# Performance work log

Hardware: AMD Instinct MI355X
Metric: run time of the kernel (lower is better)

The kernel has to match this reference:

```python
import jax, jax.numpy as jnp
import numpy as np

N_NODES = 1_000_000
N_EDGES = 16_000_000
NUM_REL = 3
C_IN, C_OUT = 3, 2


def setup_inputs() -> dict:
    key = jax.random.key(0)
    ks = jax.random.split(key, 10)
    x = jax.random.normal(ks[0], (N_NODES, C_IN), dtype=jnp.float32)
    edge_index = jax.random.randint(ks[1], (2, N_EDGES), 0, N_NODES, dtype=jnp.int64)
    edge_attr = jax.random.randint(ks[2], (N_EDGES,), 0, NUM_REL, dtype=jnp.int64)
    s = 0.3
    W1 = jax.random.normal(ks[3], (NUM_REL, C_IN, C_OUT), dtype=jnp.float32) * s
    root1 = jax.random.normal(ks[4], (C_IN, C_OUT), dtype=jnp.float32) * s
    b1 = jax.random.normal(ks[5], (C_OUT,), dtype=jnp.float32) * s
    W2 = jax.random.normal(ks[6], (NUM_REL, C_OUT, C_OUT), dtype=jnp.float32) * s
    root2 = jax.random.normal(ks[7], (C_OUT, C_OUT), dtype=jnp.float32) * s
    b2 = jax.random.normal(ks[8], (C_OUT,), dtype=jnp.float32) * s
    return {"x": x, "edge_index": edge_index, "edge_attr": edge_attr,
            "W1": W1, "root1": root1, "b1": b1,
            "W2": W2, "root2": root2, "b2": b2}


def rgcn_conv(x, edge_index, edge_type, W, root, bias, num_nodes):
    """PyG RGCNConv: per-relation mean-aggregated messages + root transform + bias."""
    src, dst = edge_index[0], edge_index[1]
    xs = x[src]                                    # [E, c_in] gather once
    out = x @ root + bias                          # [N, c_out]
    for r in range(NUM_REL):                       # small fixed relation loop
        mask = (edge_type == r)
        msg = jnp.where(mask[:, None], xs @ W[r], 0.0)          # [E, c_out]
        sums = jax.ops.segment_sum(msg, dst, num_segments=num_nodes)
        cnt = jax.ops.segment_sum(mask.astype(x.dtype), dst, num_segments=num_nodes)
        out = out + sums / jnp.maximum(cnt, 1.0)[:, None]       # mean aggr
    return out


def reference(x, edge_index, edge_attr, W1, root1, b1, W2, root2, b2):
    h = rgcn_conv(x, edge_index, edge_attr, W1, root1, b1, N_NODES)
    h = jax.nn.relu(h)
    # F.dropout(training=self.training): identity in eval mode
    out = rgcn_conv(h, edge_index, edge_attr, W2, root2, b2, N_NODES)
    return out
```

## Files before the change

### kernel.cpp

```cpp
#include <hip/hip_runtime.h>


typedef unsigned long long u64;
typedef unsigned u32;
typedef float vfloat2 __attribute__((ext_vector_type(2)));

constexpr int NN = 1000000;
constexpr int NE = 16000000;
constexpr int NR = 3;

constexpr int BSH   = 10;
constexpr int NB    = (NN + 1023) >> 10;
constexpr int BCAP  = 18432;
constexpr int EPB   = 16384;
constexpr int NBLKB = (NE + EPB - 1) / EPB;
constexpr int EPT   = EPB / 1024;

constexpr u64 M28 = (1ULL << 28) - 1;

__device__ __forceinline__ u64 pack_msg(float m0, float m1) {
    int a0 = __float2int_rn(fmaf(m0, 4096.0f, 524288.0f));
    int a1 = __float2int_rn(fmaf(m1, 4096.0f, 524288.0f));
    return (u64)(u32)a0 | ((u64)(u32)a1 << 28) | (1ULL << 56);
}

__device__ __forceinline__ u32 enc_x(float x0, float x1, float x2) {
    int q0 = __float2int_rn(fminf(fmaxf(x0 * 64.0f, -511.0f), 511.0f));
    int q1 = __float2int_rn(fminf(fmaxf(x1 * 128.0f, -1023.0f), 1023.0f));
    int q2 = __float2int_rn(fminf(fmaxf(x2 * 128.0f, -1023.0f), 1023.0f));
    return ((u32)q0 & 0x3FFu) | (((u32)q1 & 0x7FFu) << 10) | (((u32)q2 & 0x7FFu) << 21);
}

__device__ __forceinline__ void dec_x(u32 e, float& x0, float& x1, float& x2) {
    x0 = (float)((int)(e << 22) >> 22) * (1.0f / 64.0f);
    x1 = (float)((int)(e << 11) >> 21) * (1.0f / 128.0f);
    x2 = (float)((int)e >> 21)         * (1.0f / 128.0f);
}

__device__ __forceinline__ u32 enc_h(float h0, float h1) {
    int q0 = __float2int_rn(fminf(h0 * 1024.0f, 32767.0f));
    int q1 = __float2int_rn(fminf(h1 * 1024.0f, 32767.0f));
    return ((u32)q0 & 0xFFFFu) | ((u32)q1 << 16);
}

__device__ __forceinline__ void dec_h(u32 e, float& h0, float& h1) {
    h0 = (float)((int)(e << 16) >> 16) * (1.0f / 1024.0f);
    h1 = (float)((int)e >> 16)         * (1.0f / 1024.0f);
}


__global__ __launch_bounds__(1024, 8) void scatter_kernel(
    const int* __restrict__ src, const int* __restrict__ dst, const int* __restrict__ rel,
    const float* __restrict__ x, u32* __restrict__ qx,
    u32* __restrict__ buf, u32* __restrict__ cursor)
{
    __shared__ u32 stage[EPB];
    __shared__ u32 hist[1024];
    __shared__ u32 wcur[1024];
    __shared__ u32 gbase[1024];
    __shared__ u32 wt[16];
    const int tid = threadIdx.x;
    const int wave = tid >> 6, lane = tid & 63;

    hist[tid] = 0;
    __syncthreads();

    const int base = blockIdx.x * EPB;
    const int nloc = min(EPB, NE - base);

    u32 rent[EPT], rbk[EPT];
#pragma unroll
    for (int k = 0; k < EPT; ++k) {
        int i = tid + (k << 10);
        if (i < nloc) {
            int e = base + i;
            u32 d = (u32)__builtin_nontemporal_load(&dst[e]);
            u32 s = (u32)__builtin_nontemporal_load(&src[e]);
            u32 r = (u32)__builtin_nontemporal_load(&rel[e]);
            rbk[k]  = d >> BSH;
            rent[k] = s | (r << 20) | ((d & 1023u) << 22);
            atomicAdd(&hist[rbk[k]], 1u);
        }
    }
    __syncthreads();

    {
        int h0 = hist[tid];
        int v0 = h0;
#pragma unroll
        for (int d = 1; d < 64; d <<= 1) {
            int t = __shfl_up(v0, d);
            if (lane >= d) v0 += t;
        }
        if (lane == 63) wt[wave] = (u32)v0;
        __syncthreads();
        u32 off = 0;
#pragma unroll
        for (int wv = 0; wv < 16; ++wv) off += (wv < wave) ? wt[wv] : 0u;
        wcur[tid] = off + (u32)(v0 - h0);
    }
    __syncthreads();

    if (tid < NB) {
        u32 c = hist[tid];
        gbase[tid] = c ? atomicAdd(&cursor[tid], c) : 0u;
    }

    {
        int node = (blockIdx.x << BSH) + tid;
        if (node < NN)
            qx[node] = enc_x(x[3 * node + 0], x[3 * node + 1], x[3 * node + 2]);
    }
    __syncthreads();

#pragma unroll
    for (int k = 0; k < EPT; ++k) {
        int i = tid + (k << 10);
        if (i < nloc) {
            u32 sl = atomicAdd(&wcur[rbk[k]], 1u);
            stage[sl] = rent[k];
        }
    }
    __syncthreads();

    for (int b = wave; b < NB; b += 16) {
        u32 cnt = hist[b];
        if (!cnt) continue;
        u32 ls = wcur[b] - cnt;
        u32 gb = gbase[b];
        u32* bb = buf + (size_t)b * BCAP;
        for (u32 j = lane; j < cnt; j += 64) {
            u32 slot = gb + j;
            if (slot < (u32)BCAP)
                __builtin_nontemporal_store(stage[ls + j], &bb[slot]);
        }
    }
}

__global__ __launch_bounds__(512) void agg1_kernel(
    const u32* __restrict__ buf, const u32* __restrict__ cursor,
    const u32* __restrict__ qx, const float* __restrict__ x,
    const float* __restrict__ W1,
    const float* __restrict__ root1, const float* __restrict__ b1,
    u32* __restrict__ qh)
{
    __shared__ u64 acc[1024 * NR];
    __shared__ float w[NR * 3 * 2];
    const int tid = threadIdx.x;
    for (int i = tid; i < 1024 * NR; i += 512) acc[i] = 0;
    if (tid < NR * 3 * 2) w[tid] = W1[tid];
    __syncthreads();

    const int bk = blockIdx.x;
    const int n = min((int)cursor[bk], BCAP);
    const u32* bb = buf + (size_t)bk * BCAP;

    int i = tid;
    for (; i + 3584 < n; i += 4096) {
        u32 e[8], g[8];
#pragma unroll
        for (int j = 0; j < 8; ++j) e[j] = __builtin_nontemporal_load(&bb[i + 512 * j]);
#pragma unroll
        for (int j = 0; j < 8; ++j) g[j] = qx[e[j] & 0xFFFFFu];
#pragma unroll
        for (int j = 0; j < 8; ++j) {
            float a, b, c;
            dec_x(g[j], a, b, c);
            u32 r = (e[j] >> 20) & 3u; const float* wr = &w[r * 6];
            atomicAdd(&acc[(e[j] >> 22) * NR + r],
                pack_msg(a * wr[0] + b * wr[2] + c * wr[4],
                         a * wr[1] + b * wr[3] + c * wr[5]));
        }
    }
    for (; i < n; i += 512) {
        u32 e0 = __builtin_nontemporal_load(&bb[i]);
        u32 g0 = qx[e0 & 0xFFFFFu];
        float a, b, c;
        dec_x(g0, a, b, c);
        u32 r = (e0 >> 20) & 3u; const float* wr = &w[r * 6];
        atomicAdd(&acc[(e0 >> 22) * NR + r],
            pack_msg(a * wr[0] + b * wr[2] + c * wr[4],
                     a * wr[1] + b * wr[3] + c * wr[5]));
    }
    __syncthreads();

    for (int l = tid; l < 1024; l += 512) {
        int node = (bk << BSH) + l;
        if (node >= NN) continue;
        float x0 = x[3 * node + 0], x1 = x[3 * node + 1], x2 = x[3 * node + 2];
        float o0 = x0 * root1[0] + x1 * root1[2] + x2 * root1[4] + b1[0];
        float o1 = x0 * root1[1] + x1 * root1[3] + x2 * root1[5] + b1[1];
#pragma unroll
        for (int r = 0; r < NR; ++r) {
            u64 wv = acc[l * NR + r];
            int c = (int)(wv >> 56);
            int s0i = (int)(wv & M28) - (c << 19);
            int s1i = (int)((wv >> 28) & M28) - (c << 19);
            float inv = (1.0f / 4096.0f) / (float)(c > 1 ? c : 1);
            o0 += (float)s0i * inv;
            o1 += (float)s1i * inv;
        }
        qh[node] = enc_h(fmaxf(o0, 0.0f), fmaxf(o1, 0.0f));
    }
}

__global__ __launch_bounds__(512) void agg2_kernel(
    const u32* __restrict__ buf, const u32* __restrict__ cursor,
    const u32* __restrict__ qh, const float* __restrict__ W2,
    const float* __restrict__ root2, const float* __restrict__ b2,
    float* __restrict__ out)
{
    __shared__ u64 acc[1024 * NR];
    __shared__ float w[NR * 2 * 2];
    const int tid = threadIdx.x;
    for (int i = tid; i < 1024 * NR; i += 512) acc[i] = 0;
    if (tid < NR * 2 * 2) w[tid] = W2[tid];
    __syncthreads();

    const int bk = blockIdx.x;
    const int n = min((int)cursor[bk], BCAP);
    const u32* bb = buf + (size_t)bk * BCAP;

    int i = tid;
    for (; i + 3584 < n; i += 4096) {
        u32 e[8], g[8];
#pragma unroll
        for (int j = 0; j < 8; ++j) e[j] = __builtin_nontemporal_load(&bb[i + 512 * j]);
#pragma unroll
        for (int j = 0; j < 8; ++j) g[j] = qh[e[j] & 0xFFFFFu];
#pragma unroll
        for (int j = 0; j < 8; ++j) {
            float a, b;
            dec_h(g[j], a, b);
            u32 r = (e[j] >> 20) & 3u; const float* wr = &w[r * 4];
            atomicAdd(&acc[(e[j] >> 22) * NR + r],
                pack_msg(a * wr[0] + b * wr[2], a * wr[1] + b * wr[3]));
        }
    }
    for (; i < n; i += 512) {
        u32 e0 = __builtin_nontemporal_load(&bb[i]);
        u32 g0 = qh[e0 & 0xFFFFFu];
        float a, b;
        dec_h(g0, a, b);
        u32 r = (e0 >> 20) & 3u; const float* wr = &w[r * 4];
        atomicAdd(&acc[(e0 >> 22) * NR + r],
            pack_msg(a * wr[0] + b * wr[2], a * wr[1] + b * wr[3]));
    }
    __syncthreads();

    for (int l = tid; l < 1024; l += 512) {
        int node = (bk << BSH) + l;
        if (node >= NN) continue;
        float hv0, hv1;
        dec_h(qh[node], hv0, hv1);
        float o0 = hv0 * root2[0] + hv1 * root2[2] + b2[0];
        float o1 = hv0 * root2[1] + hv1 * root2[3] + b2[1];
#pragma unroll
        for (int r = 0; r < NR; ++r) {
            u64 wv = acc[l * NR + r];
            int c = (int)(wv >> 56);
            int s0i = (int)(wv & M28) - (c << 19);
            int s1i = (int)((wv >> 28) & M28) - (c << 19);
            float inv = (1.0f / 4096.0f) / (float)(c > 1 ? c : 1);
            o0 += (float)s0i * inv;
            o1 += (float)s1i * inv;
        }
        vfloat2 ov;
        ov.x = o0; ov.y = o1;
        __builtin_nontemporal_store(ov, (vfloat2*)((float2*)out + node));
    }
}


__global__ __launch_bounds__(256) void edge1_kernel(
    const int* __restrict__ src, const int* __restrict__ dst, const int* __restrict__ rel,
    const float* __restrict__ x, const float* __restrict__ W1,
    u64* __restrict__ sums1)
{
    __shared__ float w[NR * 3 * 2];
    if (threadIdx.x < NR * 3 * 2) w[threadIdx.x] = W1[threadIdx.x];
    __syncthreads();
    int e = blockIdx.x * 256 + threadIdx.x;
    if (e >= NE) return;
    int s = src[e], d = dst[e], r = rel[e];
    float x0 = x[3 * s + 0], x1 = x[3 * s + 1], x2 = x[3 * s + 2];
    const float* wr = &w[r * 6];
    float m0 = x0 * wr[0] + x1 * wr[2] + x2 * wr[4];
    float m1 = x0 * wr[1] + x1 * wr[3] + x2 * wr[5];
    atomicAdd(&sums1[d * NR + r], pack_msg(m0, m1));
}

__global__ __launch_bounds__(256) void node1_kernel(
    const float* __restrict__ x, const u64* __restrict__ sums1,
    const float* __restrict__ root1, const float* __restrict__ b1,
    float* __restrict__ h)
{
    int n = blockIdx.x * 256 + threadIdx.x;
    if (n >= NN) return;
    float x0 = x[3 * n + 0], x1 = x[3 * n + 1], x2 = x[3 * n + 2];
    float o0 = x0 * root1[0] + x1 * root1[2] + x2 * root1[4] + b1[0];
    float o1 = x0 * root1[1] + x1 * root1[3] + x2 * root1[5] + b1[1];
#pragma unroll
    for (int r = 0; r < NR; ++r) {
        u64 wv = sums1[n * NR + r];
        int c = (int)(wv >> 56);
        int s0i = (int)(wv & M28) - (c << 19);
        int s1i = (int)((wv >> 28) & M28) - (c << 19);
        float inv = (1.0f / 4096.0f) / (float)(c > 1 ? c : 1);
        o0 += (float)s0i * inv;
        o1 += (float)s1i * inv;
    }
    float2 hv;
    hv.x = fmaxf(o0, 0.0f);
    hv.y = fmaxf(o1, 0.0f);
    ((float2*)h)[n] = hv;
}

__global__ __launch_bounds__(256) void edge2_kernel(
    const int* __restrict__ src, const int* __restrict__ dst, const int* __restrict__ rel,
    const float* __restrict__ h, const float* __restrict__ W2,
    u64* __restrict__ sums2)
{
    __shared__ float w[NR * 2 * 2];
    if (threadIdx.x < NR * 2 * 2) w[threadIdx.x] = W2[threadIdx.x];
    __syncthreads();
    int e = blockIdx.x * 256 + threadIdx.x;
    if (e >= NE) return;
    int s = src[e];
    float2 hs = ((const float2*)h)[s];
    if (hs.x == 0.0f && hs.y == 0.0f) return;
    int d = dst[e], r = rel[e];
    const float* wr = &w[r * 4];
    float m0 = hs.x * wr[0] + hs.y * wr[2];
    float m1 = hs.x * wr[1] + hs.y * wr[3];
    atomicAdd(&sums2[d * NR + r], pack_msg(m0, m1));
}

__global__ __launch_bounds__(256) void node2_kernel(
    const float* __restrict__ h, const u64* __restrict__ sums1, const u64* __restrict__ sums2,
    const float* __restrict__ root2, const float* __restrict__ b2,
    float* __restrict__ out)
{
    int n = blockIdx.x * 256 + threadIdx.x;
    if (n >= NN) return;
    float2 hv = ((const float2*)h)[n];
    float o0 = hv.x * root2[0] + hv.y * root2[2] + b2[0];
    float o1 = hv.x * root2[1] + hv.y * root2[3] + b2[1];
#pragma unroll
    for (int r = 0; r < NR; ++r) {
        u64 w1 = sums1[n * NR + r];
        u64 w2 = sums2[n * NR + r];
        int c    = (int)(w1 >> 56);
        int adds = (int)(w2 >> 56);
        int s0i = (int)(w2 & M28) - (adds << 19);
        int s1i = (int)((w2 >> 28) & M28) - (adds << 19);
        float inv = (1.0f / 4096.0f) / (float)(c > 1 ? c : 1);
        o0 += (float)s0i * inv;
        o1 += (float)s1i * inv;
    }
    float2 ov; ov.x = o0; ov.y = o1;
    ((float2*)out)[n] = ov;
}

extern "C" void kernel_launch(void* const* d_in, const int* in_sizes, int n_in,
                              void* d_out, int out_size, void* d_ws, size_t ws_size,
                              hipStream_t stream) {
    const float* x     = (const float*)d_in[0];
    const int*   ei    = (const int*)d_in[1];
    const int*   rel   = (const int*)d_in[2];
    const float* W1    = (const float*)d_in[3];
    const float* root1 = (const float*)d_in[4];
    const float* b1    = (const float*)d_in[5];
    const float* W2    = (const float*)d_in[6];
    const float* root2 = (const float*)d_in[7];
    const float* b2    = (const float*)d_in[8];
    float* out = (float*)d_out;

    const int* src = ei;
    const int* dst = ei + NE;

    char* ws = (char*)d_ws;

    const size_t OFF_QX  = 72024064;
    const size_t OFF_QH  = 76024064;
    const size_t OFF_CUR = 80024064;
    const size_t WS_NEED = OFF_CUR + (size_t)NB * sizeof(u32);

    if (ws_size >= WS_NEED) {
        u32* buf    = (u32*)ws;
        u32* qx     = (u32*)(ws + OFF_QX);
        u32* qh     = (u32*)(ws + OFF_QH);
        u32* cursor = (u32*)(ws + OFF_CUR);

        hipMemsetAsync(cursor, 0, (size_t)NB * sizeof(u32), stream);
        scatter_kernel<<<NBLKB, 1024, 0, stream>>>(src, dst, rel, x, qx, buf, cursor);
        agg1_kernel<<<NB, 512, 0, stream>>>(buf, cursor, qx, x, W1, root1, b1, qh);
        agg2_kernel<<<NB, 512, 0, stream>>>(buf, cursor, qh, W2, root2, b2, out);
    } else {
        u64*   sums1 = (u64*)ws;
        u64*   sums2 = (u64*)(ws + (size_t)24 * 1000 * 1000);
        float* h     = (float*)(ws + (size_t)48 * 1000 * 1000);
        const int eb = (NE + 255) / 256;
        const int nb = (NN + 255) / 256;

        hipMemsetAsync(sums1, 0, (size_t)NN * NR * sizeof(u64), stream);
        hipMemsetAsync(sums2, 0, (size_t)NN * NR * sizeof(u64), stream);
        edge1_kernel<<<eb, 256, 0, stream>>>(src, dst, rel, x, W1, sums1);
        node1_kernel<<<nb, 256, 0, stream>>>(x, sums1, root1, b1, h);
        edge2_kernel<<<eb, 256, 0, stream>>>(src, dst, rel, h, W2, sums2);
        node2_kernel<<<nb, 256, 0, stream>>>(h, sums1, sums2, root2, b2, out);
    }
}
```

Baseline: 503.4 us.

## Fuse scatter and both aggregation stages into one cooperative persistent kernel

Replaces the three kernel launches (scatter, layer-1 aggregation, layer-2 aggregation) with a single persistent kernel of 512 blocks of 1024 threads. The stages are separated by grid-wide syncs, and each stage loops over its work items (edge chunks or node buckets). Shared memory is aliased between the scatter staging buffers and the aggregation accumulators. The aggregation phases now use 1024 threads with a 4-way unrolled gather instead of 512 threads with 8-way. The aim is to remove launch gaps and tail effects between stages. The cost is grid-sync overhead and a fixed grid that may leave fewer blocks per CU, with a three-launch fallback if the cooperative launch fails.

```diff
diff --git a/kernel.cpp b/kernel.cpp
--- a/kernel.cpp
+++ b/kernel.cpp
@@ -1,4 +1,7 @@
 #include <hip/hip_runtime.h>
+#include <hip/hip_cooperative_groups.h>
+
+namespace cg = cooperative_groups;
 
 
 typedef unsigned long long u64;
@@ -15,6 +18,7 @@
 constexpr int EPB   = 16384;
 constexpr int NBLKB = (NE + EPB - 1) / EPB;
 constexpr int EPT   = EPB / 1024;
+constexpr int GRID  = 512;
 
 constexpr u64 M28 = (1ULL << 28) - 1;
 
@@ -49,225 +53,232 @@
 }
 
 
-__global__ __launch_bounds__(1024, 8) void scatter_kernel(
+__global__ __launch_bounds__(1024, 8) void fused_kernel(
     const int* __restrict__ src, const int* __restrict__ dst, const int* __restrict__ rel,
-    const float* __restrict__ x, u32* __restrict__ qx,
-    u32* __restrict__ buf, u32* __restrict__ cursor)
+    const float* __restrict__ x,
+    const float* __restrict__ W1, const float* __restrict__ root1, const float* __restrict__ b1,
+    const float* __restrict__ W2, const float* __restrict__ root2, const float* __restrict__ b2,
+    u32* __restrict__ qx, u32* __restrict__ qh,
+    u32* __restrict__ buf, u32* __restrict__ cursor,
+    float* __restrict__ out, int mode)
 {
-    __shared__ u32 stage[EPB];
-    __shared__ u32 hist[1024];
-    __shared__ u32 wcur[1024];
-    __shared__ u32 gbase[1024];
-    __shared__ u32 wt[16];
+    __shared__ u64 smem[9736];
+    __shared__ float wsh[NR * 6];
+    u32* s32   = (u32*)smem;
+    u32* stage = s32;
+    u32* hist  = s32 + 16384;
+    u32* wcur  = s32 + 17408;
+    u32* gbase = s32 + 18432;
+    u32* wt    = s32 + 19456;
+    u64* acc   = smem;
+
     const int tid = threadIdx.x;
     const int wave = tid >> 6, lane = tid & 63;
 
-    hist[tid] = 0;
-    __syncthreads();
-
-    const int base = blockIdx.x * EPB;
-    const int nloc = min(EPB, NE - base);
-
-    u32 rent[EPT], rbk[EPT];
-#pragma unroll
-    for (int k = 0; k < EPT; ++k) {
-        int i = tid + (k << 10);
-        if (i < nloc) {
-            int e = base + i;
-            u32 d = (u32)__builtin_nontemporal_load(&dst[e]);
-            u32 s = (u32)__builtin_nontemporal_load(&src[e]);
-            u32 r = (u32)__builtin_nontemporal_load(&rel[e]);
-            rbk[k]  = d >> BSH;
-            rent[k] = s | (r << 20) | ((d & 1023u) << 22);
-            atomicAdd(&hist[rbk[k]], 1u);
+    if (mode == 0 || mode == 1) {
+        for (int c = blockIdx.x; c < NBLKB; c += gridDim.x) {
+            hist[tid] = 0;
+            __syncthreads();
+
+            const int base = c * EPB;
+            const int nloc = min(EPB, NE - base);
+
+            u32 rent[EPT], rbk[EPT];
+#pragma unroll
+            for (int k = 0; k < EPT; ++k) {
+                int i = tid + (k << 10);
+                if (i < nloc) {
+                    int e = base + i;
+                    u32 d = (u32)__builtin_nontemporal_load(&dst[e]);
+                    u32 s = (u32)__builtin_nontemporal_load(&src[e]);
+                    u32 r = (u32)__builtin_nontemporal_load(&rel[e]);
+                    rbk[k]  = d >> BSH;
+                    rent[k] = s | (r << 20) | ((d & 1023u) << 22);
+                    atomicAdd(&hist[rbk[k]], 1u);
+                }
+            }
+            __syncthreads();
+
+            {
+                int h0 = hist[tid];
+                int v0 = h0;
+#pragma unroll
+                for (int d = 1; d < 64; d <<= 1) {
+                    int t = __shfl_up(v0, d);
+                    if (lane >= d) v0 += t;
+                }
+                if (lane == 63) wt[wave] = (u32)v0;
+                __syncthreads();
+                u32 off = 0;
+#pragma unroll
+                for (int wv = 0; wv < 16; ++wv) off += (wv < wave) ? wt[wv] : 0u;
+                wcur[tid] = off + (u32)(v0 - h0);
+            }
+            __syncthreads();
+
+            if (tid < NB) {
+                u32 cc = hist[tid];
+                gbase[tid] = cc ? atomicAdd(&cursor[tid], cc) : 0u;
+            }
+
+            {
+                int node = (c << BSH) + tid;
+                if (node < NN)
+                    qx[node] = enc_x(x[3 * node + 0], x[3 * node + 1], x[3 * node + 2]);
+            }
+            __syncthreads();
+
+#pragma unroll
+            for (int k = 0; k < EPT; ++k) {
+                int i = tid + (k << 10);
+                if (i < nloc) {
+                    u32 sl = atomicAdd(&wcur[rbk[k]], 1u);
+                    stage[sl] = rent[k];
+                }
+            }
+            __syncthreads();
+
+            for (int b = wave; b < NB; b += 16) {
+                u32 cnt = hist[b];
+                if (!cnt) continue;
+                u32 ls = wcur[b] - cnt;
+                u32 gb = gbase[b];
+                u32* bb = buf + (size_t)b * BCAP;
+                for (u32 j = lane; j < cnt; j += 64) {
+                    u32 slot = gb + j;
+                    if (slot < (u32)BCAP)
+                        __builtin_nontemporal_store(stage[ls + j], &bb[slot]);
+                }
+            }
+            __syncthreads();
         }
     }
-    __syncthreads();
-
-    {
-        int h0 = hist[tid];
-        int v0 = h0;
-#pragma unroll
-        for (int d = 1; d < 64; d <<= 1) {
-            int t = __shfl_up(v0, d);
-            if (lane >= d) v0 += t;
+
+    if (mode == 0) cg::this_grid().sync();
+
+    if (mode == 0 || mode == 2) {
+        if (tid < NR * 6) wsh[tid] = W1[tid];
+        for (int b = blockIdx.x; b < NB; b += gridDim.x) {
+            for (int i2 = tid; i2 < 1024 * NR; i2 += 1024) acc[i2] = 0;
+            __syncthreads();
+
+            const int n = min((int)cursor[b], BCAP);
+            const u32* bb = buf + (size_t)b * BCAP;
+
+            int i = tid;
+            for (; i + 3072 < n; i += 4096) {
+                u32 e[4], g[4];
+#pragma unroll
+                for (int j = 0; j < 4; ++j) e[j] = __builtin_nontemporal_load(&bb[i + 1024 * j]);
+#pragma unroll
+                for (int j = 0; j < 4; ++j) g[j] = qx[e[j] & 0xFFFFFu];
+#pragma unroll
+                for (int j = 0; j < 4; ++j) {
+                    float a, bfl, cfl;
+                    dec_x(g[j], a, bfl, cfl);
+                    u32 r = (e[j] >> 20) & 3u; const float* wr = &wsh[r * 6];
+                    atomicAdd(&acc[(e[j] >> 22) * NR + r],
+                        pack_msg(a * wr[0] + bfl * wr[2] + cfl * wr[4],
+                                 a * wr[1] + bfl * wr[3] + cfl * wr[5]));
+                }
+            }
+            for (; i < n; i += 1024) {
+                u32 e0 = __builtin_nontemporal_load(&bb[i]);
+                u32 g0 = qx[e0 & 0xFFFFFu];
+                float a, bfl, cfl;
+                dec_x(g0, a, bfl, cfl);
+                u32 r = (e0 >> 20) & 3u; const float* wr = &wsh[r * 6];
+                atomicAdd(&acc[(e0 >> 22) * NR + r],
+                    pack_msg(a * wr[0] + bfl * wr[2] + cfl * wr[4],
+                             a * wr[1] + bfl * wr[3] + cfl * wr[5]));
+            }
+            __syncthreads();
+
+            {
+                int node = (b << BSH) + tid;
+                if (node < NN) {
+                    float x0 = x[3 * node + 0], x1 = x[3 * node + 1], x2 = x[3 * node + 2];
+                    float o0 = x0 * root1[0] + x1 * root1[2] + x2 * root1[4] + b1[0];
+                    float o1 = x0 * root1[1] + x1 * root1[3] + x2 * root1[5] + b1[1];
+#pragma unroll
+                    for (int r = 0; r < NR; ++r) {
+                        u64 wv = acc[tid * NR + r];
+                        int c2 = (int)(wv >> 56);
+                        int s0i = (int)(wv & M28) - (c2 << 19);
+                        int s1i = (int)((wv >> 28) & M28) - (c2 << 19);
+                        float inv = (1.0f / 4096.0f) / (float)(c2 > 1 ? c2 : 1);
+                        o0 += (float)s0i * inv;
+                        o1 += (float)s1i * inv;
+                    }
+                    qh[node] = enc_h(fmaxf(o0, 0.0f), fmaxf(o1, 0.0f));
+                }
+            }
+            __syncthreads();
         }
-        if (lane == 63) wt[wave] = (u32)v0;
-        __syncthreads();
-        u32 off = 0;
-#pragma unroll
-        for (int wv = 0; wv < 16; ++wv) off += (wv < wave) ? wt[wv] : 0u;
-        wcur[tid] = off + (u32)(v0 - h0);
-    }
-    __syncthreads();
-
-    if (tid < NB) {
-        u32 c = hist[tid];
-        gbase[tid] = c ? atomicAdd(&cursor[tid], c) : 0u;
-    }
-
-    {
-        int node = (blockIdx.x << BSH) + tid;
-        if (node < NN)
-            qx[node] = enc_x(x[3 * node + 0], x[3 * node + 1], x[3 * node + 2]);
-    }
-    __syncthreads();
-
-#pragma unroll
-    for (int k = 0; k < EPT; ++k) {
-        int i = tid + (k << 10);
-        if (i < nloc) {
-            u32 sl = atomicAdd(&wcur[rbk[k]], 1u);
-            stage[sl] = rent[k];
+    }
+
+    if (mode == 0) cg::this_grid().sync();
+
+    if (mode == 0 || mode == 3) {
+        if (tid < NR * 4) wsh[tid] = W2[tid];
+        for (int b = blockIdx.x; b < NB; b += gridDim.x) {
+            for (int i2 = tid; i2 < 1024 * NR; i2 += 1024) acc[i2] = 0;
+            __syncthreads();
+
+            const int n = min((int)cursor[b], BCAP);
+            const u32* bb = buf + (size_t)b * BCAP;
+
+            int i = tid;
+            for (; i + 3072 < n; i += 4096) {
+                u32 e[4], g[4];
+#pragma unroll
+                for (int j = 0; j < 4; ++j) e[j] = __builtin_nontemporal_load(&bb[i + 1024 * j]);
+#pragma unroll
+                for (int j = 0; j < 4; ++j) g[j] = qh[e[j] & 0xFFFFFu];
+#pragma unroll
+                for (int j = 0; j < 4; ++j) {
+                    float a, bfl;
+                    dec_h(g[j], a, bfl);
+                    u32 r = (e[j] >> 20) & 3u; const float* wr = &wsh[r * 4];
+                    atomicAdd(&acc[(e[j] >> 22) * NR + r],
+                        pack_msg(a * wr[0] + bfl * wr[2], a * wr[1] + bfl * wr[3]));
+                }
+            }
+            for (; i < n; i += 1024) {
+                u32 e0 = __builtin_nontemporal_load(&bb[i]);
+                u32 g0 = qh[e0 & 0xFFFFFu];
+                float a, bfl;
+                dec_h(g0, a, bfl);
+                u32 r = (e0 >> 20) & 3u; const float* wr = &wsh[r * 4];
+                atomicAdd(&acc[(e0 >> 22) * NR + r],
+                    pack_msg(a * wr[0] + bfl * wr[2], a * wr[1] + bfl * wr[3]));
+            }
+            __syncthreads();
+
+            {
+                int node = (b << BSH) + tid;
+                if (node < NN) {
+                    float hv0, hv1;
+                    dec_h(qh[node], hv0, hv1);
+                    float o0 = hv0 * root2[0] + hv1 * root2[2] + b2[0];
+                    float o1 = hv0 * root2[1] + hv1 * root2[3] + b2[1];
+#pragma unroll
+                    for (int r = 0; r < NR; ++r) {
+                        u64 wv = acc[tid * NR + r];
+                        int c2 = (int)(wv >> 56);
+                        int s0i = (int)(wv & M28) - (c2 << 19);
+                        int s1i = (int)((wv >> 28) & M28) - (c2 << 19);
+                        float inv = (1.0f / 4096.0f) / (float)(c2 > 1 ? c2 : 1);
+                        o0 += (float)s0i * inv;
+                        o1 += (float)s1i * inv;
+                    }
+                    vfloat2 ov;
+                    ov.x = o0; ov.y = o1;
+                    __builtin_nontemporal_store(ov, (vfloat2*)((float2*)out + node));
+                }
+            }
+            __syncthreads();
         }
-    }
-    __syncthreads();
-
-    for (int b = wave; b < NB; b += 16) {
-        u32 cnt = hist[b];
-        if (!cnt) continue;
-        u32 ls = wcur[b] - cnt;
-        u32 gb = gbase[b];
-        u32* bb = buf + (size_t)b * BCAP;
-        for (u32 j = lane; j < cnt; j += 64) {
-            u32 slot = gb + j;
-            if (slot < (u32)BCAP)
-                __builtin_nontemporal_store(stage[ls + j], &bb[slot]);
-        }
-    }
-}
-
-__global__ __launch_bounds__(512) void agg1_kernel(
-    const u32* __restrict__ buf, const u32* __restrict__ cursor,
-    const u32* __restrict__ qx, const float* __restrict__ x,
-    const float* __restrict__ W1,
-    const float* __restrict__ root1, const float* __restrict__ b1,
-    u32* __restrict__ qh)
-{
-    __shared__ u64 acc[1024 * NR];
-    __shared__ float w[NR * 3 * 2];
-    const int tid = threadIdx.x;
-    for (int i = tid; i < 1024 * NR; i += 512) acc[i] = 0;
-    if (tid < NR * 3 * 2) w[tid] = W1[tid];
-    __syncthreads();
-
-    const int bk = blockIdx.x;
-    const int n = min((int)cursor[bk], BCAP);
-    const u32* bb = buf + (size_t)bk * BCAP;
-
-    int i = tid;
-    for (; i + 3584 < n; i += 4096) {
-        u32 e[8], g[8];
-#pragma unroll
-        for (int j = 0; j < 8; ++j) e[j] = __builtin_nontemporal_load(&bb[i + 512 * j]);
-#pragma unroll
-        for (int j = 0; j < 8; ++j) g[j] = qx[e[j] & 0xFFFFFu];
-#pragma unroll
-        for (int j = 0; j < 8; ++j) {
-            float a, b, c;
-            dec_x(g[j], a, b, c);
-            u32 r = (e[j] >> 20) & 3u; const float* wr = &w[r * 6];
-            atomicAdd(&acc[(e[j] >> 22) * NR + r],
-                pack_msg(a * wr[0] + b * wr[2] + c * wr[4],
-                         a * wr[1] + b * wr[3] + c * wr[5]));
-        }
-    }
-    for (; i < n; i += 512) {
-        u32 e0 = __builtin_nontemporal_load(&bb[i]);
-        u32 g0 = qx[e0 & 0xFFFFFu];
-        float a, b, c;
-        dec_x(g0, a, b, c);
-        u32 r = (e0 >> 20) & 3u; const float* wr = &w[r * 6];
-        atomicAdd(&acc[(e0 >> 22) * NR + r],
-            pack_msg(a * wr[0] + b * wr[2] + c * wr[4],
-                     a * wr[1] + b * wr[3] + c * wr[5]));
-    }
-    __syncthreads();
-
-    for (int l = tid; l < 1024; l += 512) {
-        int node = (bk << BSH) + l;
-        if (node >= NN) continue;
-        float x0 = x[3 * node + 0], x1 = x[3 * node + 1], x2 = x[3 * node + 2];
-        float o0 = x0 * root1[0] + x1 * root1[2] + x2 * root1[4] + b1[0];
-        float o1 = x0 * root1[1] + x1 * root1[3] + x2 * root1[5] + b1[1];
-#pragma unroll
-        for (int r = 0; r < NR; ++r) {
-            u64 wv = acc[l * NR + r];
-            int c = (int)(wv >> 56);
-            int s0i = (int)(wv & M28) - (c << 19);
-            int s1i = (int)((wv >> 28) & M28) - (c << 19);
-            float inv = (1.0f / 4096.0f) / (float)(c > 1 ? c : 1);
-            o0 += (float)s0i * inv;
-            o1 += (float)s1i * inv;
-        }
-        qh[node] = enc_h(fmaxf(o0, 0.0f), fmaxf(o1, 0.0f));
-    }
-}
-
-__global__ __launch_bounds__(512) void agg2_kernel(
-    const u32* __restrict__ buf, const u32* __restrict__ cursor,
-    const u32* __restrict__ qh, const float* __restrict__ W2,
-    const float* __restrict__ root2, const float* __restrict__ b2,
-    float* __restrict__ out)
-{
-    __shared__ u64 acc[1024 * NR];
-    __shared__ float w[NR * 2 * 2];
-    const int tid = threadIdx.x;
-    for (int i = tid; i < 1024 * NR; i += 512) acc[i] = 0;
-    if (tid < NR * 2 * 2) w[tid] = W2[tid];
-    __syncthreads();
-
-    const int bk = blockIdx.x;
-    const int n = min((int)cursor[bk], BCAP);
-    const u32* bb = buf + (size_t)bk * BCAP;
-
-    int i = tid;
-    for (; i + 3584 < n; i += 4096) {
-        u32 e[8], g[8];
-#pragma unroll
-        for (int j = 0; j < 8; ++j) e[j] = __builtin_nontemporal_load(&bb[i + 512 * j]);
-#pragma unroll
-        for (int j = 0; j < 8; ++j) g[j] = qh[e[j] & 0xFFFFFu];
-#pragma unroll
-        for (int j = 0; j < 8; ++j) {
-            float a, b;
-            dec_h(g[j], a, b);
-            u32 r = (e[j] >> 20) & 3u; const float* wr = &w[r * 4];
-            atomicAdd(&acc[(e[j] >> 22) * NR + r],
-                pack_msg(a * wr[0] + b * wr[2], a * wr[1] + b * wr[3]));
-        }
-    }
-    for (; i < n; i += 512) {
-        u32 e0 = __builtin_nontemporal_load(&bb[i]);
-        u32 g0 = qh[e0 & 0xFFFFFu];
-        float a, b;
-        dec_h(g0, a, b);
-        u32 r = (e0 >> 20) & 3u; const float* wr = &w[r * 4];
-        atomicAdd(&acc[(e0 >> 22) * NR + r],
-            pack_msg(a * wr[0] + b * wr[2], a * wr[1] + b * wr[3]));
-    }
-    __syncthreads();
-
-    for (int l = tid; l < 1024; l += 512) {
-        int node = (bk << BSH) + l;
-        if (node >= NN) continue;
-        float hv0, hv1;
-        dec_h(qh[node], hv0, hv1);
-        float o0 = hv0 * root2[0] + hv1 * root2[2] + b2[0];
-        float o1 = hv0 * root2[1] + hv1 * root2[3] + b2[1];
-#pragma unroll
-        for (int r = 0; r < NR; ++r) {
-            u64 wv = acc[l * NR + r];
-            int c = (int)(wv >> 56);
-            int s0i = (int)(wv & M28) - (c << 19);
-            int s1i = (int)((wv >> 28) & M28) - (c << 19);
-            float inv = (1.0f / 4096.0f) / (float)(c > 1 ? c : 1);
-            o0 += (float)s0i * inv;
-            o1 += (float)s1i * inv;
-        }
-        vfloat2 ov;
-        ov.x = o0; ov.y = o1;
-        __builtin_nontemporal_store(ov, (vfloat2*)((float2*)out + node));
     }
 }
 
@@ -393,9 +404,25 @@
         u32* cursor = (u32*)(ws + OFF_CUR);
 
         hipMemsetAsync(cursor, 0, (size_t)NB * sizeof(u32), stream);
-        scatter_kernel<<<NBLKB, 1024, 0, stream>>>(src, dst, rel, x, qx, buf, cursor);
-        agg1_kernel<<<NB, 512, 0, stream>>>(buf, cursor, qx, x, W1, root1, b1, qh);
-        agg2_kernel<<<NB, 512, 0, stream>>>(buf, cursor, qh, W2, root2, b2, out);
+
+        int mode = 0;
+        void* kargs[] = {
+            (void*)&src, (void*)&dst, (void*)&rel, (void*)&x,
+            (void*)&W1, (void*)&root1, (void*)&b1,
+            (void*)&W2, (void*)&root2, (void*)&b2,
+            (void*)&qx, (void*)&qh, (void*)&buf, (void*)&cursor,
+            (void*)&out, (void*)&mode
+        };
+        hipError_t cerr = hipLaunchCooperativeKernel(
+            (const void*)fused_kernel, dim3(GRID), dim3(1024), kargs, 0, stream);
+        if (cerr != hipSuccess) {
+            fused_kernel<<<GRID, 1024, 0, stream>>>(src, dst, rel, x,
+                W1, root1, b1, W2, root2, b2, qx, qh, buf, cursor, out, 1);
+            fused_kernel<<<GRID, 1024, 0, stream>>>(src, dst, rel, x,
+                W1, root1, b1, W2, root2, b2, qx, qh, buf, cursor, out, 2);
+            fused_kernel<<<GRID, 1024, 0, stream>>>(src, dst, rel, x,
+                W1, root1, b1, W2, root2, b2, qx, qh, buf, cursor, out, 3);
+        }
     } else {
         u64*   sums1 = (u64*)ws;
         u64*   sums2 = (u64*)(ws + (size_t)24 * 1000 * 1000);
```

Result: slower. 657.7 us (+30.7%).
